# Kernel optimization log

Hardware: AMD Instinct MI355X
Metric: run time of the kernel (lower is better)

The kernel has to match this reference:

```python
import jax, jax.numpy as jnp
import numpy as np

B, L, C, H, HH, NL, O = 4096, 512, 8, 64, 128, 3, 1  # batch, time length, input/hidden/hidden_hidden chans, layers, out


def _lin(k, i, o):
    s = 1.0 / np.sqrt(i)
    return jax.random.uniform(k, (i, o), jnp.float32, -s, s)


def setup_inputs():
    key = jax.random.key(0)
    ks = jax.random.split(key, 8)
    return {
        "coeffs": jax.random.normal(ks[0], (B, L - 1, 4 * C), jnp.float32) * 0.1,
        "W_init": _lin(ks[1], C, H), "b_init": jnp.zeros((H,), jnp.float32),
        "W_in": _lin(ks[2], H, HH), "b_in": jnp.zeros((HH,), jnp.float32),
        "W_h": jnp.stack([_lin(ks[3 + i], HH, HH) for i in range(NL - 1)]),
        "b_h": jnp.zeros((NL - 1, HH), jnp.float32),
        "W_out": _lin(ks[5], HH, C * H), "b_out": jnp.zeros((C * H,), jnp.float32),
        "W_read": _lin(ks[6], H, O), "b_read": jnp.zeros((O,), jnp.float32),
    }


def _cde_func(z, W_in, b_in, W_h, b_h, W_out, b_out):
    # CDEFunc MLP: (B,H) -> (B,H,C)
    h = jax.nn.relu(z @ W_in + b_in)
    for i in range(W_h.shape[0]):
        h = jax.nn.relu(h @ W_h[i] + b_h[i])
    f = jnp.tanh(h @ W_out + b_out)
    return f.reshape(z.shape[0], H, C)


def reference(coeffs, W_init, b_init, W_in, b_in, W_h, b_h, W_out, b_out, W_read, b_read):
    # torchcde.CubicSpline coeffs layout: cat([a, b, two_c, three_d], dim=-1)
    a, bb, two_c, three_d = jnp.split(coeffs, 4, axis=-1)  # each (B, L-1, C)
    # X(interval[0]) = a of the first segment (fractional part 0)
    z = a[:, 0, :] @ W_init + b_init  # (B, H)
    # grid_points = arange(L); step size h = 1 between consecutive grid points
    bs = jnp.moveaxis(bb, 1, 0)       # (L-1, B, C)
    cs = jnp.moveaxis(two_c, 1, 0)
    ds = jnp.moveaxis(three_d, 1, 0)

    def step(z, seg):
        bn, cn, dn = seg
        deriv = lambda frac: bn + (cn + dn * frac) * frac  # dX/dt within segment
        g = lambda zz, dX: jnp.einsum(
            'bhc,bc->bh', _cde_func(zz, W_in, b_in, W_h, b_h, W_out, b_out), dX)
        third = jnp.float32(1.0 / 3.0)
        # torchdiffeq 'rk4' fixed-grid solver = Kutta's 3/8 rule (rk4_alt_step_func), h=1
        k1 = g(z, deriv(0.0))
        k2 = g(z + k1 * third, deriv(third))
        k3 = g(z + (k2 - k1 * third), deriv(2.0 * third))
        k4 = g(z + (k1 - k2 + k3), deriv(1.0))
        z = z + (k1 + 3.0 * (k2 + k3) + k4) * jnp.float32(0.125)
        return z, None

    zT, _ = jax.lax.scan(step, z, (bs, cs, ds))  # final hidden state z(T)
    return zT @ W_read + b_read  # (B, O)
```

## Files before the change

kernel.cpp:

```cpp
#include <hip/hip_runtime.h>
#include <stdint.h>

typedef short s16x8 __attribute__((ext_vector_type(8)));
typedef float f32x4 __attribute__((ext_vector_type(4)));

#define LSEG 511

static __device__ __forceinline__ uint32_t cvt_pk_bf16(float lo, float hi) {
  uint32_t r;
  asm("v_cvt_pk_bf16_f32 %0, %1, %2" : "=v"(r) : "v"(lo), "v"(hi));
  return r;
}
static __device__ __forceinline__ unsigned short f2bf(float f) {
  union { float f; uint32_t u; } v; v.f = f;
  uint32_t r = (v.u + 0x7FFFu + ((v.u >> 16) & 1u)) >> 16;
  return (unsigned short)r;
}
static __device__ __forceinline__ float tanh_fast(float x) {
  float ex = __expf(2.f * x);
  return 1.f - 2.f * __builtin_amdgcn_rcpf(ex + 1.f);
}
static __device__ __forceinline__ float dpp_xor8(float x) {
  return __int_as_float(__builtin_amdgcn_update_dpp(
      0, __float_as_int(x), 0x128, 0xF, 0xF, false));
}

__global__ __attribute__((amdgpu_flat_work_group_size(512, 512),
                          amdgpu_waves_per_eu(2, 2)))
void cde_kernel(
    const float* __restrict__ coeffs,
    const float* __restrict__ W_init, const float* __restrict__ b_init,
    const float* __restrict__ W_in,  const float* __restrict__ b_in,
    const float* __restrict__ W_h,   const float* __restrict__ b_h,
    const float* __restrict__ W_out, const float* __restrict__ b_out,
    const float* __restrict__ W_read,const float* __restrict__ b_read,
    float* __restrict__ out)
{
  __shared__ __align__(16) char H1mem[16 * 256];
  __shared__ __align__(16) char H2mem[16 * 256];
  __shared__ __align__(16) char Xmem[16 * 128];
  __shared__ float dx2[4][2][16][4];

  const int tid  = threadIdx.x;
  const int w    = tid >> 6;
  const int lane = tid & 63;
  const int lr   = lane & 15;
  const int lk   = lane >> 4;
  const int lc   = lr & 7;
  const int hp   = lr >> 3;
  const int b0   = blockIdx.x * 16;
  const int h_own = 8*w + lc;

  s16x8 Win_f[2], Wh0_f[4], Wh1_f[4], Wout_f[4][4];
  const int wc = 16*w + lr;
  #pragma unroll
  for (int kq = 0; kq < 2; ++kq)
    #pragma unroll
    for (int e = 0; e < 8; ++e)
      Win_f[kq][e] = (short)f2bf(W_in[(32*kq + 8*lk + e)*128 + wc]);
  #pragma unroll
  for (int kq = 0; kq < 4; ++kq)
    #pragma unroll
    for (int e = 0; e < 8; ++e) {
      Wh0_f[kq][e] = (short)f2bf(W_h[(32*kq + 8*lk + e)*128 + wc]);
      Wh1_f[kq][e] = (short)f2bf(W_h[16384 + (32*kq + 8*lk + e)*128 + wc]);
    }
  #pragma unroll
  for (int kq = 0; kq < 4; ++kq)
    #pragma unroll
    for (int nt = 0; nt < 4; ++nt) {
      const int ch = 64*w + 8*lc + 2*nt + hp;
      #pragma unroll
      for (int e = 0; e < 8; ++e)
        Wout_f[kq][nt][e] = (short)f2bf(W_out[(32*kq + 8*lk + e)*512 + ch]);
    }
  const float binv = b_in[wc];
  const float bh0v = b_h[wc];
  const float bh1v = b_h[128 + wc];
  const f32x4 bin4 = {binv, binv, binv, binv};
  const f32x4 bh04 = {bh0v, bh0v, bh0v, bh0v};
  const f32x4 bh14 = {bh1v, bh1v, bh1v, bh1v};
  f32x4 bout4[4];
  #pragma unroll
  for (int nt = 0; nt < 4; ++nt) {
    const float b = b_out[64*w + 8*lc + 2*nt + hp];
    bout4[nt] = (f32x4){b, b, b, b};
  }

  const int r2  = (lr >> 2) & 1;
  const int vbHe = lr*256 + (((lk ^ lr) & 3) << 4) + (r2 << 6);
  const int vbHo = lr*256 + (((lk ^ lr) & 3) << 4) + ((1 ^ r2) << 6);
  const int vbX0 = lr*128 + ((lk ^ (lr & 7)) << 4);
  const int vbX1 = vbX0 ^ 64;
  int wbH[4];
  #pragma unroll
  for (int r = 0; r < 4; ++r) {
    const int row = 4*lk + r;
    wbH[r] = row*256 + ((((2*w + (lr >> 3)) ^ (row & 7)) << 4)) + ((lr & 7) << 1);
  }
  int wbX[2];
  #pragma unroll
  for (int j = 0; j < 2; ++j) {
    const int ro = 4*lk + 2*hp + j;
    wbX[j] = ro*128 + (((w ^ (ro & 7)) << 4)) + (lc << 1);
  }
  const int dbx = hp*256 + (lk << 6);

  float z0[2], zfin[2], k1r[2], k2r[2];
  {
    float Wi[8];
    #pragma unroll
    for (int c = 0; c < 8; ++c) Wi[c] = W_init[c*64 + h_own];
    const float bi = b_init[h_own];
    #pragma unroll
    for (int j = 0; j < 2; ++j) {
      const int ro = 4*lk + 2*hp + j;
      const float* a0r = &coeffs[(size_t)(b0 + ro) * (LSEG*32)];
      float s = bi;
      #pragma unroll
      for (int c = 0; c < 8; ++c) s = fmaf(a0r[c], Wi[c], s);
      z0[j] = s; zfin[j] = 0.f; k1r[j] = 0.f; k2r[j] = 0.f;
      *(unsigned short*)(Xmem + wbX[j]) = f2bf(s);
    }
  }

  float cf_b = 0.f, cf_c = 0.f, cf_d = 0.f;
  const int crow = 2*w + (lane >> 5), ccc = (lane >> 2) & 7;
  const bool cact = (lane & 3) == 0;
  if (cact) {
    const float* cp = &coeffs[(size_t)(b0 + crow)*(LSEG*32)];
    cf_b = cp[8+ccc]; cf_c = cp[16+ccc]; cf_d = cp[24+ccc];
  }
  __syncthreads();

  #pragma unroll 1
  for (int t = 0; t < LSEG; ++t) {
    #pragma unroll
    for (int s = 0; s < 4; ++s) {
      if (s == 0 && cact) {
        const float third = 1.f/3.f, two3 = 2.f/3.f;
        const int dxo = (ccc & 1)*256 + crow*16 + (ccc >> 1)*4;
        *(float*)((char*)dx2 + dxo)        = cf_b;
        *(float*)((char*)dx2 + dxo + 512)  = fmaf(fmaf(cf_d, third, cf_c), third, cf_b);
        *(float*)((char*)dx2 + dxo + 1024) = fmaf(fmaf(cf_d, two3, cf_c), two3, cf_b);
        *(float*)((char*)dx2 + dxo + 1536) = cf_b + cf_c + cf_d;
        if (t + 1 < LSEG) {
          const float* cp = &coeffs[((size_t)(b0 + crow)*LSEG + (t+1))*32];
          cf_b = cp[8+ccc]; cf_c = cp[16+ccc]; cf_d = cp[24+ccc];
        }
      }
      {
        s16x8 a0 = *(const s16x8*)(Xmem + vbX0);
        s16x8 a1 = *(const s16x8*)(Xmem + vbX1);
        f32x4 acc;
        acc = __builtin_amdgcn_mfma_f32_16x16x32_bf16(a0, Win_f[0], bin4, 0, 0, 0);
        acc = __builtin_amdgcn_mfma_f32_16x16x32_bf16(a1, Win_f[1], acc, 0, 0, 0);
        #pragma unroll
        for (int r = 0; r < 4; ++r) {
          float v = fmaxf(acc[r], 0.f);
          *(unsigned short*)(H1mem + wbH[r]) = (unsigned short)cvt_pk_bf16(v, v);
        }
      }
      __syncthreads();

      {
        s16x8 a0 = *(const s16x8*)(H1mem + vbHe);
        s16x8 a1 = *(const s16x8*)(H1mem + vbHo);
        s16x8 a2 = *(const s16x8*)(H1mem + vbHe + 128);
        s16x8 a3 = *(const s16x8*)(H1mem + vbHo + 128);
        f32x4 acc0, acc1 = {};
        acc0 = __builtin_amdgcn_mfma_f32_16x16x32_bf16(a0, Wh0_f[0], bh04, 0, 0, 0);
        acc1 = __builtin_amdgcn_mfma_f32_16x16x32_bf16(a1, Wh0_f[1], acc1, 0, 0, 0);
        acc0 = __builtin_amdgcn_mfma_f32_16x16x32_bf16(a2, Wh0_f[2], acc0, 0, 0, 0);
        acc1 = __builtin_amdgcn_mfma_f32_16x16x32_bf16(a3, Wh0_f[3], acc1, 0, 0, 0);
        f32x4 acc = acc0 + acc1;
        #pragma unroll
        for (int r = 0; r < 4; ++r) {
          float v = fmaxf(acc[r], 0.f);
          *(unsigned short*)(H2mem + wbH[r]) = (unsigned short)cvt_pk_bf16(v, v);
        }
      }
      __syncthreads();

      {
        s16x8 a0 = *(const s16x8*)(H2mem + vbHe);
        s16x8 a1 = *(const s16x8*)(H2mem + vbHo);
        s16x8 a2 = *(const s16x8*)(H2mem + vbHe + 128);
        s16x8 a3 = *(const s16x8*)(H2mem + vbHo + 128);
        f32x4 acc0, acc1 = {};
        acc0 = __builtin_amdgcn_mfma_f32_16x16x32_bf16(a0, Wh1_f[0], bh14, 0, 0, 0);
        acc1 = __builtin_amdgcn_mfma_f32_16x16x32_bf16(a1, Wh1_f[1], acc1, 0, 0, 0);
        acc0 = __builtin_amdgcn_mfma_f32_16x16x32_bf16(a2, Wh1_f[2], acc0, 0, 0, 0);
        acc1 = __builtin_amdgcn_mfma_f32_16x16x32_bf16(a3, Wh1_f[3], acc1, 0, 0, 0);
        f32x4 acc = acc0 + acc1;
        #pragma unroll
        for (int r = 0; r < 4; ++r) {
          float v = fmaxf(acc[r], 0.f);
          *(unsigned short*)(H1mem + wbH[r]) = (unsigned short)cvt_pk_bf16(v, v);
        }
      }
      __syncthreads();

      {
        f32x4 dxv[4];
        #pragma unroll
        for (int r = 0; r < 4; ++r)
          dxv[r] = *(const f32x4*)((char*)dx2 + dbx + s*512 + r*16);
        s16x8 a0 = *(const s16x8*)(H1mem + vbHe);
        s16x8 a1 = *(const s16x8*)(H1mem + vbHo);
        s16x8 a2 = *(const s16x8*)(H1mem + vbHe + 128);
        s16x8 a3 = *(const s16x8*)(H1mem + vbHo + 128);
        f32x4 acc[4];
        #pragma unroll
        for (int nt = 0; nt < 4; ++nt)
          acc[nt] = __builtin_amdgcn_mfma_f32_16x16x32_bf16(a0, Wout_f[0][nt], bout4[nt], 0, 0, 0);
        #pragma unroll
        for (int nt = 0; nt < 4; ++nt)
          acc[nt] = __builtin_amdgcn_mfma_f32_16x16x32_bf16(a1, Wout_f[1][nt], acc[nt], 0, 0, 0);
        #pragma unroll
        for (int nt = 0; nt < 4; ++nt)
          acc[nt] = __builtin_amdgcn_mfma_f32_16x16x32_bf16(a2, Wout_f[2][nt], acc[nt], 0, 0, 0);
        #pragma unroll
        for (int nt = 0; nt < 4; ++nt)
          acc[nt] = __builtin_amdgcn_mfma_f32_16x16x32_bf16(a3, Wout_f[3][nt], acc[nt], 0, 0, 0);
        float sums[4];
        #pragma unroll
        for (int r = 0; r < 4; ++r) {
          float sum = 0.f;
          #pragma unroll
          for (int nt = 0; nt < 4; ++nt)
            sum = fmaf(tanh_fast(acc[nt][r]), dxv[r][nt], sum);
          sums[r] = sum + dpp_xor8(sum);
        }
        #pragma unroll
        for (int j = 0; j < 2; ++j) {
          const float sum = sums[2*hp + j];
          float znext;
          if (s == 0) {
            k1r[j] = sum;
            zfin[j] = fmaf(0.125f, sum, z0[j]);
            znext   = fmaf(1.f/3.f, sum, z0[j]);
          } else if (s == 1) {
            k2r[j] = sum;
            zfin[j] = fmaf(0.375f, sum, zfin[j]);
            znext   = z0[j] + sum - (1.f/3.f)*k1r[j];
          } else if (s == 2) {
            zfin[j] = fmaf(0.375f, sum, zfin[j]);
            znext   = z0[j] + k1r[j] - k2r[j] + sum;
          } else {
            zfin[j] = fmaf(0.125f, sum, zfin[j]);
            znext   = zfin[j];
            z0[j]   = zfin[j];
          }
          *(unsigned short*)(Xmem + wbX[j]) = (unsigned short)cvt_pk_bf16(znext, znext);
        }
      }
      __syncthreads();
    }
  }

  float* ZF = (float*)H1mem;
  #pragma unroll
  for (int j = 0; j < 2; ++j)
    ZF[(4*lk + 2*hp + j)*64 + h_own] = z0[j];
  __syncthreads();
  if (tid < 16) {
    float acc = b_read[0];
    for (int h = 0; h < 64; ++h) acc = fmaf(ZF[tid*64 + h], W_read[h], acc);
    out[b0 + tid] = acc;
  }
}

extern "C" void kernel_launch(void* const* d_in, const int* in_sizes, int n_in,
                              void* d_out, int out_size, void* d_ws, size_t ws_size,
                              hipStream_t stream) {
  const float* coeffs = (const float*)d_in[0];
  const float* W_init = (const float*)d_in[1];
  const float* b_init = (const float*)d_in[2];
  const float* W_in   = (const float*)d_in[3];
  const float* b_in   = (const float*)d_in[4];
  const float* W_h    = (const float*)d_in[5];
  const float* b_h    = (const float*)d_in[6];
  const float* W_out  = (const float*)d_in[7];
  const float* b_out  = (const float*)d_in[8];
  const float* W_read = (const float*)d_in[9];
  const float* b_read = (const float*)d_in[10];
  float* out = (float*)d_out;

  cde_kernel<<<dim3(256), dim3(512), 0, stream>>>(
      coeffs, W_init, b_init, W_in, b_in, W_h, b_h, W_out, b_out,
      W_read, b_read, out);
}
```

Measured before the change: 2.988 ms.

## Specialize waves: four for hidden MLP layers, four for output layer

Splits the eight waves into two roles. Waves 0-3 compute the input and hidden layers, two output tiles each. Waves 4-3+4 compute the wide W_out layer, the tanh-weighted contraction and the RK state update. Before, every wave did a slice of every layer. The intent is to hold more weight fragments per wave in registers and balance the large output GEMM against the smaller hidden layers. The catch is that within each barrier-separated stage half the waves sit idle, so per-step latency could rise unless the MFMA units were underused.

```diff
diff --git a/kernel.cpp b/kernel.cpp
--- a/kernel.cpp
+++ b/kernel.cpp
@@ -49,84 +49,91 @@
   const int lc   = lr & 7;
   const int hp   = lr >> 3;
   const int b0   = blockIdx.x * 16;
-  const int h_own = 8*w + lc;
-
-  s16x8 Win_f[2], Wh0_f[4], Wh1_f[4], Wout_f[4][4];
-  const int wc = 16*w + lr;
-  #pragma unroll
-  for (int kq = 0; kq < 2; ++kq)
-    #pragma unroll
-    for (int e = 0; e < 8; ++e)
-      Win_f[kq][e] = (short)f2bf(W_in[(32*kq + 8*lk + e)*128 + wc]);
+  const bool isOut = w >= 4;
+  const int ow   = w & 3;
+
+  s16x8 WF[32];
+  f32x4 bin4[2], bh04[2], bh14[2];
+  float boutS[8];
+  if (!isOut) {
+    #pragma unroll
+    for (int nt = 0; nt < 2; ++nt) {
+      const int col = 32*ow + 16*nt + lr;
+      #pragma unroll
+      for (int kq = 0; kq < 2; ++kq)
+        #pragma unroll
+        for (int e = 0; e < 8; ++e)
+          WF[kq*2+nt][e] = (short)f2bf(W_in[(32*kq + 8*lk + e)*128 + col]);
+      #pragma unroll
+      for (int kq = 0; kq < 4; ++kq)
+        #pragma unroll
+        for (int e = 0; e < 8; ++e) {
+          WF[4+kq*2+nt][e]  = (short)f2bf(W_h[(32*kq + 8*lk + e)*128 + col]);
+          WF[12+kq*2+nt][e] = (short)f2bf(W_h[16384 + (32*kq + 8*lk + e)*128 + col]);
+        }
+      const float b1 = b_in[col], b2 = b_h[col], b3 = b_h[128 + col];
+      bin4[nt] = (f32x4){b1, b1, b1, b1};
+      bh04[nt] = (f32x4){b2, b2, b2, b2};
+      bh14[nt] = (f32x4){b3, b3, b3, b3};
+    }
+  } else {
+    #pragma unroll
+    for (int nt = 0; nt < 8; ++nt) {
+      const int ch = 128*ow + 16*lc + (nt >> 2)*8 + 2*(nt & 3) + hp;
+      #pragma unroll
+      for (int kq = 0; kq < 4; ++kq)
+        #pragma unroll
+        for (int e = 0; e < 8; ++e)
+          WF[kq*8+nt][e] = (short)f2bf(W_out[(32*kq + 8*lk + e)*512 + ch]);
+      boutS[nt] = b_out[ch];
+    }
+  }
+
+  int vb[4];
   #pragma unroll
   for (int kq = 0; kq < 4; ++kq)
-    #pragma unroll
-    for (int e = 0; e < 8; ++e) {
-      Wh0_f[kq][e] = (short)f2bf(W_h[(32*kq + 8*lk + e)*128 + wc]);
-      Wh1_f[kq][e] = (short)f2bf(W_h[16384 + (32*kq + 8*lk + e)*128 + wc]);
-    }
+    vb[kq] = lr*256 + (((4*kq + lk) ^ (lr & 15)) << 4);
+  const int vbX0 = lr*128 + ((lk ^ lc) << 4);
+  const int vbX1 = vbX0 ^ 64;
+  int wbH[2][4];
   #pragma unroll
-  for (int kq = 0; kq < 4; ++kq)
-    #pragma unroll
-    for (int nt = 0; nt < 4; ++nt) {
-      const int ch = 64*w + 8*lc + 2*nt + hp;
-      #pragma unroll
-      for (int e = 0; e < 8; ++e)
-        Wout_f[kq][nt][e] = (short)f2bf(W_out[(32*kq + 8*lk + e)*512 + ch]);
-    }
-  const float binv = b_in[wc];
-  const float bh0v = b_h[wc];
-  const float bh1v = b_h[128 + wc];
-  const f32x4 bin4 = {binv, binv, binv, binv};
-  const f32x4 bh04 = {bh0v, bh0v, bh0v, bh0v};
-  const f32x4 bh14 = {bh1v, bh1v, bh1v, bh1v};
-  f32x4 bout4[4];
-  #pragma unroll
-  for (int nt = 0; nt < 4; ++nt) {
-    const float b = b_out[64*w + 8*lc + 2*nt + hp];
-    bout4[nt] = (f32x4){b, b, b, b};
-  }
-
-  const int r2  = (lr >> 2) & 1;
-  const int vbHe = lr*256 + (((lk ^ lr) & 3) << 4) + (r2 << 6);
-  const int vbHo = lr*256 + (((lk ^ lr) & 3) << 4) + ((1 ^ r2) << 6);
-  const int vbX0 = lr*128 + ((lk ^ (lr & 7)) << 4);
-  const int vbX1 = vbX0 ^ 64;
-  int wbH[4];
-  #pragma unroll
-  for (int r = 0; r < 4; ++r) {
-    const int row = 4*lk + r;
-    wbH[r] = row*256 + ((((2*w + (lr >> 3)) ^ (row & 7)) << 4)) + ((lr & 7) << 1);
-  }
-  int wbX[2];
+  for (int nt = 0; nt < 2; ++nt)
+    #pragma unroll
+    for (int r = 0; r < 4; ++r) {
+      const int row = 4*lk + r;
+      wbH[nt][r] = row*256 + ((((4*ow + 2*nt + hp) ^ (row & 15)) << 4)) + 2*lc;
+    }
+  int wbX32[2];
   #pragma unroll
   for (int j = 0; j < 2; ++j) {
     const int ro = 4*lk + 2*hp + j;
-    wbX[j] = ro*128 + (((w ^ (ro & 7)) << 4)) + (lc << 1);
-  }
-  const int dbx = hp*256 + (lk << 6);
-
-  float z0[2], zfin[2], k1r[2], k2r[2];
-  {
-    float Wi[8];
-    #pragma unroll
-    for (int c = 0; c < 8; ++c) Wi[c] = W_init[c*64 + h_own];
-    const float bi = b_init[h_own];
+    wbX32[j] = ro*128 + (((2*ow + (lc >> 2)) ^ (ro & 7)) << 4) + 4*(lc & 3);
+  }
+  const int dbx = hp*256 + lk*64;
+
+  float z0[2][2], zfin[2][2], k1r[2][2], k2r[2][2];
+  if (isOut) {
     #pragma unroll
     for (int j = 0; j < 2; ++j) {
       const int ro = 4*lk + 2*hp + j;
       const float* a0r = &coeffs[(size_t)(b0 + ro) * (LSEG*32)];
-      float s = bi;
-      #pragma unroll
-      for (int c = 0; c < 8; ++c) s = fmaf(a0r[c], Wi[c], s);
-      z0[j] = s; zfin[j] = 0.f; k1r[j] = 0.f; k2r[j] = 0.f;
-      *(unsigned short*)(Xmem + wbX[j]) = f2bf(s);
+      #pragma unroll
+      for (int m = 0; m < 2; ++m) {
+        const int h = 16*ow + 2*lc + m;
+        float sv = b_init[h];
+        #pragma unroll
+        for (int c = 0; c < 8; ++c) sv = fmaf(a0r[c], W_init[c*64 + h], sv);
+        z0[j][m] = sv; zfin[j][m] = 0.f; k1r[j][m] = 0.f; k2r[j][m] = 0.f;
+      }
+      *(uint32_t*)(Xmem + wbX32[j]) = cvt_pk_bf16(z0[j][0], z0[j][1]);
     }
   }
 
   float cf_b = 0.f, cf_c = 0.f, cf_d = 0.f;
-  const int crow = 2*w + (lane >> 5), ccc = (lane >> 2) & 7;
-  const bool cact = (lane & 3) == 0;
+  const int cidx = lane >> 1;
+  const int crow = 4*ow + (cidx >> 3);
+  const int ccc  = cidx & 7;
+  const bool cact = (!isOut) && ((lane & 1) == 0);
   if (cact) {
     const float* cp = &coeffs[(size_t)(b0 + crow)*(LSEG*32)];
     cf_b = cp[8+ccc]; cf_c = cp[16+ccc]; cf_d = cp[24+ccc];
@@ -137,122 +144,146 @@
   for (int t = 0; t < LSEG; ++t) {
     #pragma unroll
     for (int s = 0; s < 4; ++s) {
-      if (s == 0 && cact) {
-        const float third = 1.f/3.f, two3 = 2.f/3.f;
-        const int dxo = (ccc & 1)*256 + crow*16 + (ccc >> 1)*4;
-        *(float*)((char*)dx2 + dxo)        = cf_b;
-        *(float*)((char*)dx2 + dxo + 512)  = fmaf(fmaf(cf_d, third, cf_c), third, cf_b);
-        *(float*)((char*)dx2 + dxo + 1024) = fmaf(fmaf(cf_d, two3, cf_c), two3, cf_b);
-        *(float*)((char*)dx2 + dxo + 1536) = cf_b + cf_c + cf_d;
-        if (t + 1 < LSEG) {
-          const float* cp = &coeffs[((size_t)(b0 + crow)*LSEG + (t+1))*32];
-          cf_b = cp[8+ccc]; cf_c = cp[16+ccc]; cf_d = cp[24+ccc];
-        }
-      }
-      {
+      if (!isOut) {
+        if (s == 0 && cact) {
+          const float third = 1.f/3.f, two3 = 2.f/3.f;
+          const int dxo = (ccc & 1)*256 + crow*16 + (ccc >> 1)*4;
+          *(float*)((char*)dx2 + dxo)        = cf_b;
+          *(float*)((char*)dx2 + dxo + 512)  = fmaf(fmaf(cf_d, third, cf_c), third, cf_b);
+          *(float*)((char*)dx2 + dxo + 1024) = fmaf(fmaf(cf_d, two3, cf_c), two3, cf_b);
+          *(float*)((char*)dx2 + dxo + 1536) = cf_b + cf_c + cf_d;
+          if (t + 1 < LSEG) {
+            const float* cp = &coeffs[((size_t)(b0 + crow)*LSEG + (t+1))*32];
+            cf_b = cp[8+ccc]; cf_c = cp[16+ccc]; cf_d = cp[24+ccc];
+          }
+        }
         s16x8 a0 = *(const s16x8*)(Xmem + vbX0);
         s16x8 a1 = *(const s16x8*)(Xmem + vbX1);
-        f32x4 acc;
-        acc = __builtin_amdgcn_mfma_f32_16x16x32_bf16(a0, Win_f[0], bin4, 0, 0, 0);
-        acc = __builtin_amdgcn_mfma_f32_16x16x32_bf16(a1, Win_f[1], acc, 0, 0, 0);
-        #pragma unroll
-        for (int r = 0; r < 4; ++r) {
-          float v = fmaxf(acc[r], 0.f);
-          *(unsigned short*)(H1mem + wbH[r]) = (unsigned short)cvt_pk_bf16(v, v);
+        #pragma unroll
+        for (int nt = 0; nt < 2; ++nt) {
+          f32x4 acc = __builtin_amdgcn_mfma_f32_16x16x32_bf16(a0, WF[nt],   bin4[nt], 0, 0, 0);
+          acc       = __builtin_amdgcn_mfma_f32_16x16x32_bf16(a1, WF[2+nt], acc,      0, 0, 0);
+          #pragma unroll
+          for (int r = 0; r < 4; ++r) {
+            float v = fmaxf(acc[r], 0.f);
+            *(unsigned short*)(H1mem + wbH[nt][r]) = (unsigned short)cvt_pk_bf16(v, v);
+          }
         }
       }
       __syncthreads();
 
-      {
-        s16x8 a0 = *(const s16x8*)(H1mem + vbHe);
-        s16x8 a1 = *(const s16x8*)(H1mem + vbHo);
-        s16x8 a2 = *(const s16x8*)(H1mem + vbHe + 128);
-        s16x8 a3 = *(const s16x8*)(H1mem + vbHo + 128);
-        f32x4 acc0, acc1 = {};
-        acc0 = __builtin_amdgcn_mfma_f32_16x16x32_bf16(a0, Wh0_f[0], bh04, 0, 0, 0);
-        acc1 = __builtin_amdgcn_mfma_f32_16x16x32_bf16(a1, Wh0_f[1], acc1, 0, 0, 0);
-        acc0 = __builtin_amdgcn_mfma_f32_16x16x32_bf16(a2, Wh0_f[2], acc0, 0, 0, 0);
-        acc1 = __builtin_amdgcn_mfma_f32_16x16x32_bf16(a3, Wh0_f[3], acc1, 0, 0, 0);
-        f32x4 acc = acc0 + acc1;
-        #pragma unroll
-        for (int r = 0; r < 4; ++r) {
-          float v = fmaxf(acc[r], 0.f);
-          *(unsigned short*)(H2mem + wbH[r]) = (unsigned short)cvt_pk_bf16(v, v);
+      if (!isOut) {
+        s16x8 a0 = *(const s16x8*)(H1mem + vb[0]);
+        s16x8 a1 = *(const s16x8*)(H1mem + vb[1]);
+        s16x8 a2 = *(const s16x8*)(H1mem + vb[2]);
+        s16x8 a3 = *(const s16x8*)(H1mem + vb[3]);
+        #pragma unroll
+        for (int nt = 0; nt < 2; ++nt) {
+          f32x4 acc = __builtin_amdgcn_mfma_f32_16x16x32_bf16(a0, WF[4+nt],  bh04[nt], 0, 0, 0);
+          acc       = __builtin_amdgcn_mfma_f32_16x16x32_bf16(a1, WF[6+nt],  acc, 0, 0, 0);
+          acc       = __builtin_amdgcn_mfma_f32_16x16x32_bf16(a2, WF[8+nt],  acc, 0, 0, 0);
+          acc       = __builtin_amdgcn_mfma_f32_16x16x32_bf16(a3, WF[10+nt], acc, 0, 0, 0);
+          #pragma unroll
+          for (int r = 0; r < 4; ++r) {
+            float v = fmaxf(acc[r], 0.f);
+            *(unsigned short*)(H2mem + wbH[nt][r]) = (unsigned short)cvt_pk_bf16(v, v);
+          }
         }
       }
       __syncthreads();
 
-      {
-        s16x8 a0 = *(const s16x8*)(H2mem + vbHe);
-        s16x8 a1 = *(const s16x8*)(H2mem + vbHo);
-        s16x8 a2 = *(const s16x8*)(H2mem + vbHe + 128);
-        s16x8 a3 = *(const s16x8*)(H2mem + vbHo + 128);
-        f32x4 acc0, acc1 = {};
-        acc0 = __builtin_amdgcn_mfma_f32_16x16x32_bf16(a0, Wh1_f[0], bh14, 0, 0, 0);
-        acc1 = __builtin_amdgcn_mfma_f32_16x16x32_bf16(a1, Wh1_f[1], acc1, 0, 0, 0);
-        acc0 = __builtin_amdgcn_mfma_f32_16x16x32_bf16(a2, Wh1_f[2], acc0, 0, 0, 0);
-        acc1 = __builtin_amdgcn_mfma_f32_16x16x32_bf16(a3, Wh1_f[3], acc1, 0, 0, 0);
-        f32x4 acc = acc0 + acc1;
-        #pragma unroll
-        for (int r = 0; r < 4; ++r) {
-          float v = fmaxf(acc[r], 0.f);
-          *(unsigned short*)(H1mem + wbH[r]) = (unsigned short)cvt_pk_bf16(v, v);
+      if (!isOut) {
+        s16x8 a0 = *(const s16x8*)(H2mem + vb[0]);
+        s16x8 a1 = *(const s16x8*)(H2mem + vb[1]);
+        s16x8 a2 = *(const s16x8*)(H2mem + vb[2]);
+        s16x8 a3 = *(const s16x8*)(H2mem + vb[3]);
+        #pragma unroll
+        for (int nt = 0; nt < 2; ++nt) {
+          f32x4 acc = __builtin_amdgcn_mfma_f32_16x16x32_bf16(a0, WF[12+nt], bh14[nt], 0, 0, 0);
+          acc       = __builtin_amdgcn_mfma_f32_16x16x32_bf16(a1, WF[14+nt], acc, 0, 0, 0);
+          acc       = __builtin_amdgcn_mfma_f32_16x16x32_bf16(a2, WF[16+nt], acc, 0, 0, 0);
+          acc       = __builtin_amdgcn_mfma_f32_16x16x32_bf16(a3, WF[18+nt], acc, 0, 0, 0);
+          #pragma unroll
+          for (int r = 0; r < 4; ++r) {
+            float v = fmaxf(acc[r], 0.f);
+            *(unsigned short*)(H1mem + wbH[nt][r]) = (unsigned short)cvt_pk_bf16(v, v);
+          }
         }
       }
       __syncthreads();
 
-      {
+      if (isOut) {
         f32x4 dxv[4];
         #pragma unroll
         for (int r = 0; r < 4; ++r)
-          dxv[r] = *(const f32x4*)((char*)dx2 + dbx + s*512 + r*16);
-        s16x8 a0 = *(const s16x8*)(H1mem + vbHe);
-        s16x8 a1 = *(const s16x8*)(H1mem + vbHo);
-        s16x8 a2 = *(const s16x8*)(H1mem + vbHe + 128);
-        s16x8 a3 = *(const s16x8*)(H1mem + vbHo + 128);
-        f32x4 acc[4];
-        #pragma unroll
-        for (int nt = 0; nt < 4; ++nt)
-          acc[nt] = __builtin_amdgcn_mfma_f32_16x16x32_bf16(a0, Wout_f[0][nt], bout4[nt], 0, 0, 0);
-        #pragma unroll
-        for (int nt = 0; nt < 4; ++nt)
-          acc[nt] = __builtin_amdgcn_mfma_f32_16x16x32_bf16(a1, Wout_f[1][nt], acc[nt], 0, 0, 0);
-        #pragma unroll
-        for (int nt = 0; nt < 4; ++nt)
-          acc[nt] = __builtin_amdgcn_mfma_f32_16x16x32_bf16(a2, Wout_f[2][nt], acc[nt], 0, 0, 0);
-        #pragma unroll
-        for (int nt = 0; nt < 4; ++nt)
-          acc[nt] = __builtin_amdgcn_mfma_f32_16x16x32_bf16(a3, Wout_f[3][nt], acc[nt], 0, 0, 0);
-        float sums[4];
-        #pragma unroll
-        for (int r = 0; r < 4; ++r) {
-          float sum = 0.f;
-          #pragma unroll
-          for (int nt = 0; nt < 4; ++nt)
-            sum = fmaf(tanh_fast(acc[nt][r]), dxv[r][nt], sum);
-          sums[r] = sum + dpp_xor8(sum);
+          dxv[r] = *(const f32x4*)((const char*)dx2 + dbx + s*512 + r*16);
+        s16x8 a0 = *(const s16x8*)(H1mem + vb[0]);
+        s16x8 a1 = *(const s16x8*)(H1mem + vb[1]);
+        s16x8 a2 = *(const s16x8*)(H1mem + vb[2]);
+        s16x8 a3 = *(const s16x8*)(H1mem + vb[3]);
+        const f32x4 fz = {0.f, 0.f, 0.f, 0.f};
+        float sumA[4], sumB[4];
+        {
+          f32x4 acc[4];
+          #pragma unroll
+          for (int nt = 0; nt < 4; ++nt) {
+            f32x4 tacc = __builtin_amdgcn_mfma_f32_16x16x32_bf16(a0, WF[nt],    fz,   0, 0, 0);
+            tacc       = __builtin_amdgcn_mfma_f32_16x16x32_bf16(a1, WF[8+nt],  tacc, 0, 0, 0);
+            tacc       = __builtin_amdgcn_mfma_f32_16x16x32_bf16(a2, WF[16+nt], tacc, 0, 0, 0);
+            acc[nt]    = __builtin_amdgcn_mfma_f32_16x16x32_bf16(a3, WF[24+nt], tacc, 0, 0, 0);
+          }
+          #pragma unroll
+          for (int r = 0; r < 4; ++r) {
+            float sv = 0.f;
+            #pragma unroll
+            for (int nt = 0; nt < 4; ++nt)
+              sv = fmaf(tanh_fast(acc[nt][r] + boutS[nt]), dxv[r][nt], sv);
+            sumA[r] = sv + dpp_xor8(sv);
+          }
+        }
+        {
+          f32x4 acc[4];
+          #pragma unroll
+          for (int nt = 0; nt < 4; ++nt) {
+            f32x4 tacc = __builtin_amdgcn_mfma_f32_16x16x32_bf16(a0, WF[4+nt],  fz,   0, 0, 0);
+            tacc       = __builtin_amdgcn_mfma_f32_16x16x32_bf16(a1, WF[12+nt], tacc, 0, 0, 0);
+            tacc       = __builtin_amdgcn_mfma_f32_16x16x32_bf16(a2, WF[20+nt], tacc, 0, 0, 0);
+            acc[nt]    = __builtin_amdgcn_mfma_f32_16x16x32_bf16(a3, WF[28+nt], tacc, 0, 0, 0);
+          }
+          #pragma unroll
+          for (int r = 0; r < 4; ++r) {
+            float sv = 0.f;
+            #pragma unroll
+            for (int nt = 0; nt < 4; ++nt)
+              sv = fmaf(tanh_fast(acc[nt][r] + boutS[4+nt]), dxv[r][nt], sv);
+            sumB[r] = sv + dpp_xor8(sv);
+          }
         }
         #pragma unroll
         for (int j = 0; j < 2; ++j) {
-          const float sum = sums[2*hp + j];
-          float znext;
-          if (s == 0) {
-            k1r[j] = sum;
-            zfin[j] = fmaf(0.125f, sum, z0[j]);
-            znext   = fmaf(1.f/3.f, sum, z0[j]);
-          } else if (s == 1) {
-            k2r[j] = sum;
-            zfin[j] = fmaf(0.375f, sum, zfin[j]);
-            znext   = z0[j] + sum - (1.f/3.f)*k1r[j];
-          } else if (s == 2) {
-            zfin[j] = fmaf(0.375f, sum, zfin[j]);
-            znext   = z0[j] + k1r[j] - k2r[j] + sum;
-          } else {
-            zfin[j] = fmaf(0.125f, sum, zfin[j]);
-            znext   = zfin[j];
-            z0[j]   = zfin[j];
-          }
-          *(unsigned short*)(Xmem + wbX[j]) = (unsigned short)cvt_pk_bf16(znext, znext);
+          float zn[2];
+          #pragma unroll
+          for (int m = 0; m < 2; ++m) {
+            const float s0 = hp ? (m ? sumB[2+j] : sumA[2+j])
+                                : (m ? sumB[j]   : sumA[j]);
+            if (s == 0) {
+              k1r[j][m] = s0;
+              zfin[j][m] = fmaf(0.125f, s0, z0[j][m]);
+              zn[m]      = fmaf(1.f/3.f, s0, z0[j][m]);
+            } else if (s == 1) {
+              k2r[j][m] = s0;
+              zfin[j][m] = fmaf(0.375f, s0, zfin[j][m]);
+              zn[m]      = z0[j][m] + s0 - (1.f/3.f)*k1r[j][m];
+            } else if (s == 2) {
+              zfin[j][m] = fmaf(0.375f, s0, zfin[j][m]);
+              zn[m]      = z0[j][m] + k1r[j][m] - k2r[j][m] + s0;
+            } else {
+              zfin[j][m] = fmaf(0.125f, s0, zfin[j][m]);
+              zn[m]      = zfin[j][m];
+              z0[j][m]   = zfin[j][m];
+            }
+          }
+          *(uint32_t*)(Xmem + wbX32[j]) = cvt_pk_bf16(zn[0], zn[1]);
         }
       }
       __syncthreads();
@@ -260,9 +291,13 @@
   }
 
   float* ZF = (float*)H1mem;
-  #pragma unroll
-  for (int j = 0; j < 2; ++j)
-    ZF[(4*lk + 2*hp + j)*64 + h_own] = z0[j];
+  if (isOut) {
+    #pragma unroll
+    for (int j = 0; j < 2; ++j)
+      #pragma unroll
+      for (int m = 0; m < 2; ++m)
+        ZF[(4*lk + 2*hp + j)*64 + 16*ow + 2*lc + m] = z0[j][m];
+  }
   __syncthreads();
   if (tid < 16) {
     float acc = b_read[0];
```

Result: slower. 4.095 ms (+37.1%).
